# Kernel optimization log

Hardware: AMD Instinct MI355X
Metric: run time of the kernel (lower is better)

The kernel has to match this reference:

```python
import jax, jax.numpy as jnp
import numpy as np

NEG_SLOPE = 0.01  # nn.LeakyReLU default
NUM_GRAPHS = 64


def leaky_relu(x):
    return jnp.where(x >= 0, x, NEG_SLOPE * x)


def gcn_conv(x, edge_index, W, b):
    """PyG GCNConv: add self-loops, symmetric norm, aggregate, + bias."""
    n = x.shape[0]
    h = x @ W  # [N, F]
    loop = jnp.arange(n, dtype=edge_index.dtype)
    src = jnp.concatenate([edge_index[0], loop])
    dst = jnp.concatenate([edge_index[1], loop])
    deg = jax.ops.segment_sum(jnp.ones_like(dst, dtype=h.dtype), dst, num_segments=n)
    dinv = jnp.where(deg > 0, deg ** -0.5, 0.0)
    norm = dinv[src] * dinv[dst]  # [E+N]
    msg = h[src] * norm[:, None]  # [E+N, F] dominant intermediate
    out = jax.ops.segment_sum(msg, dst, num_segments=n)
    return out + b


def gep(x, batch, num_graphs):
    """global mean pool over batch segment ids."""
    s = jax.ops.segment_sum(x, batch, num_segments=num_graphs)
    cnt = jax.ops.segment_sum(jnp.ones(x.shape[0], dtype=x.dtype), batch, num_segments=num_graphs)
    return s / jnp.maximum(cnt, 1.0)[:, None]


def setup_inputs() -> dict:
    key = jax.random.key(0)
    ks = jax.random.split(key, 16)
    N, E, F, D, B = 10000, 80000, 1024, 128, NUM_GRAPHS
    sc = 1.0 / np.sqrt(F)
    inp = {
        "pro1_x": jax.random.normal(ks[0], (N, F), jnp.float32),
        "pro1_edge_index": jax.random.randint(ks[1], (2, E), 0, N, jnp.int64),
        "pro1_batch": jnp.sort(jax.random.randint(ks[2], (N,), 0, B, jnp.int64)),
        "pro2_x": jax.random.normal(ks[3], (N, F), jnp.float32),
        "pro2_edge_index": jax.random.randint(ks[4], (2, E), 0, N, jnp.int64),
        "pro2_batch": jnp.sort(jax.random.randint(ks[5], (N,), 0, B, jnp.int64)),
        "mas1_straight": 0, "mas1_flipped": 0, "mas2_straight": 0, "mas2_flipped": 0,
        "conv1_W": jax.random.normal(ks[6], (F, F), jnp.float32) * sc,
        "conv1_b": jnp.zeros((F,), jnp.float32),
        "fc1_W": jax.random.normal(ks[7], (F, D), jnp.float32) * sc,
        "fc1_b": jnp.zeros((D,), jnp.float32),
        "conv2_W": jax.random.normal(ks[8], (F, F), jnp.float32) * sc,
        "conv2_b": jnp.zeros((F,), jnp.float32),
        "fc2_W": jax.random.normal(ks[9], (F, D), jnp.float32) * sc,
        "fc2_b": jnp.zeros((D,), jnp.float32),
        "final_W": jax.random.normal(ks[10], (2 * D, 1), jnp.float32) * (1.0 / np.sqrt(2 * D)),
        "final_b": jnp.zeros((1,), jnp.float32),
    }
    return inp


def reference(pro1_x, pro1_edge_index, pro1_batch, pro2_x, pro2_edge_index, pro2_batch,
              mas1_straight, mas1_flipped, mas2_straight, mas2_flipped,
              conv1_W, conv1_b, fc1_W, fc1_b, conv2_W, conv2_b, fc2_W, fc2_b,
              final_W, final_b):
    # branch 1 (dropout = identity at inference)
    x = leaky_relu(gcn_conv(pro1_x, pro1_edge_index, conv1_W, conv1_b))
    x = gep(x, pro1_batch, NUM_GRAPHS)
    x = leaky_relu(x @ fc1_W + fc1_b)
    # branch 2
    xt = leaky_relu(gcn_conv(pro2_x, pro2_edge_index, conv2_W, conv2_b))
    xt = gep(xt, pro2_batch, NUM_GRAPHS)
    xt = leaky_relu(xt @ fc2_W + fc2_b)
    combined = jnp.concatenate([x, xt], axis=1)  # [B, 256]
    return combined @ final_W + final_b  # [B, 1]
```

## Files before the change

kernel.cpp:

```cpp
#include <hip/hip_runtime.h>
#include <cstdint>
#include <cstddef>

#define FDIM 1024
#define DDIM 128
#define NGRAPH 64
#define FCH 8
#define QN 4
#define FILLB 320

#define AS1 __attribute__((address_space(1)))
#define AS3 __attribute__((address_space(3)))

typedef float f32x4 __attribute__((ext_vector_type(4)));
typedef short s16x8 __attribute__((ext_vector_type(8)));

__device__ __forceinline__ unsigned short f2bf(float f) {
  unsigned int x = __float_as_uint(f);
  unsigned int r = (x + 0x7fffu + ((x >> 16) & 1u)) >> 16;
  return (unsigned short)r;
}
__device__ __forceinline__ float bflo(unsigned int v) {
  return __uint_as_float(v << 16);
}
__device__ __forceinline__ float bfhi(unsigned int v) {
  return __uint_as_float(v & 0xffff0000u);
}

__device__ __forceinline__ int lower_bound(const int* a, int n, int v) {
  int lo = 0, hi = n;
  while (lo < hi) {
    int mid = (lo + hi) >> 1;
    if (a[mid] < v) lo = mid + 1; else hi = mid;
  }
  return lo;
}
__global__ __launch_bounds__(256) void k_init(int* deg1, int* deg2,
                                              const int* __restrict__ batch1,
                                              const int* __restrict__ batch2,
                                              int* cnt1, int* gstart1,
                                              int* cnt2, int* gstart2, int N) {
  int bid = blockIdx.x, t = threadIdx.x;
  if (bid < 40) {
    int i = bid * 256 + t;
    if (i < N) deg1[i] = 1;
  } else if (bid < 80) {
    int i = (bid - 40) * 256 + t;
    if (i < N) deg2[i] = 1;
  } else {
    if (t < 128) {
      const int* batch = (t < NGRAPH) ? batch1 : batch2;
      int* cnt = (t < NGRAPH) ? cnt1 : cnt2;
      int* gstart = (t < NGRAPH) ? gstart1 : gstart2;
      int g = t & (NGRAPH - 1);
      int lo = lower_bound(batch, N, g);
      int hi = lower_bound(batch, N, g + 1);
      gstart[g] = lo;
      cnt[g] = hi - lo;
    }
  }
}

__global__ __launch_bounds__(256) void k_prep_cast(const int* __restrict__ ei1,
                                                   const int* __restrict__ ei2,
                                                   int* deg1, int* deg2,
                                                   const float4* __restrict__ x1,
                                                   const float4* __restrict__ x2,
                                                   const float* __restrict__ W1,
                                                   const float* __restrict__ W2,
                                                   ushort4* xb1, ushort4* xb2,
                                                   unsigned short* Wt1, unsigned short* Wt2,
                                                   int E, int n4, int gE, int nxb) {
  __shared__ unsigned short tile[64][65];
  int br = blockIdx.y;
  int x = blockIdx.x, t = threadIdx.x;
  if (x < gE) {
    const int* ei = br ? ei2 : ei1;
    int* deg = br ? deg2 : deg1;
    int i = x * 256 + t;
    if (i < E) atomicAdd(&deg[ei[E + i]], 1);
  } else if (x < gE + nxb) {
    const float4* xx = br ? x2 : x1;
    ushort4* xb = br ? xb2 : xb1;
    int i = (x - gE) * 256 + t;
    if (i < n4) {
      float4 v = xx[i];
      ushort4 o;
      o.x = f2bf(v.x); o.y = f2bf(v.y); o.z = f2bf(v.z); o.w = f2bf(v.w);
      xb[i] = o;
    }
  } else {
    const float* W = br ? W2 : W1;
    unsigned short* Wt = br ? Wt2 : Wt1;
    int tid16 = x - gE - nxb;
    int kb = tid16 >> 4, nb = tid16 & 15;
    int tn = t & 63, tg = t >> 6;
    #pragma unroll
    for (int r = 0; r < 16; ++r) {
      int kk = tg * 16 + r;
      tile[kk][tn] = f2bf(W[(size_t)(kb * 64 + kk) * FDIM + nb * 64 + tn]);
    }
    __syncthreads();
    #pragma unroll
    for (int r = 0; r < 16; ++r) {
      int nn = tg * 16 + r;
      Wt[(size_t)(nb * 64 + nn) * FDIM + kb * 64 + tn] = tile[tn][nn];
    }
  }
}

#define SCAN_T 1024
#define SCAN_PER 16
__global__ __launch_bounds__(SCAN_T) void k_scan(const int* __restrict__ deg1,
                                                 const int* __restrict__ deg2,
                                                 int* off1, int* off2,
                                                 int* cur1, int* cur2,
                                                 float* dinv1, float* dinv2, int n) {
  const int* deg = blockIdx.x ? deg2 : deg1;
  int* off = blockIdx.x ? off2 : off1;
  int* cur = blockIdx.x ? cur2 : cur1;
  float* dinv = blockIdx.x ? dinv2 : dinv1;
  __shared__ int sums[SCAN_T];
  int t = threadIdx.x;
  int base = t * SCAN_PER;
  int local[SCAN_PER];
  int s = 0;
  #pragma unroll
  for (int i = 0; i < SCAN_PER; ++i) {
    int idx = base + i;
    int d = (idx < n) ? deg[idx] : 0;
    local[i] = s;
    s += d;
    if (idx < n) dinv[idx] = rsqrtf((float)d);
  }
  sums[t] = s;
  __syncthreads();
  for (int o = 1; o < SCAN_T; o <<= 1) {
    int v = (t >= o) ? sums[t - o] : 0;
    __syncthreads();
    sums[t] += v;
    __syncthreads();
  }
  int basesum = (t > 0) ? sums[t - 1] : 0;
  #pragma unroll
  for (int i = 0; i < SCAN_PER; ++i) {
    int idx = base + i;
    if (idx < n) { int o = basesum + local[i]; off[idx] = o; cur[idx] = o; }
  }
  if (t == SCAN_T - 1) off[n] = sums[SCAN_T - 1];
}

__global__ __launch_bounds__(256) void k_fill_gemm(const int* __restrict__ ei1,
                                                   const int* __restrict__ ei2,
                                                   int* cur1, int* cur2,
                                                   const float* __restrict__ dinv1,
                                                   const float* __restrict__ dinv2,
                                                   int* adjsrc1, int* adjsrc2,
                                                   float* adjw1, float* adjw2,
                                                   const unsigned short* __restrict__ A1,
                                                   const unsigned short* __restrict__ A2,
                                                   const unsigned short* __restrict__ B1,
                                                   const unsigned short* __restrict__ B2,
                                                   unsigned short* __restrict__ C1,
                                                   unsigned short* __restrict__ C2,
                                                   int E, int N, int M) {
  __shared__ unsigned short sm[8192];
  int br = blockIdx.y;
  if (blockIdx.x < FILLB) {
    const int* ei = br ? ei2 : ei1;
    int* cur = br ? cur2 : cur1;
    const float* dinv = br ? dinv2 : dinv1;
    int* adjsrc = br ? adjsrc2 : adjsrc1;
    float* adjw = br ? adjw2 : adjw1;
    int i = blockIdx.x * 256 + threadIdx.x;
    if (i < E) {
      int s = ei[i];
      int d = ei[E + i];
      int p = atomicAdd(&cur[d], 1);
      adjsrc[p] = s;
      adjw[p] = dinv[s] * dinv[d];
    }
    if (i < N) {
      int p = atomicAdd(&cur[i], 1);
      adjsrc[p] = i;
      adjw[p] = dinv[i] * dinv[i];
    }
    return;
  }
  const unsigned short* A = br ? A2 : A1;
  const unsigned short* Bt = br ? B2 : B1;
  unsigned short* C = br ? C2 : C1;
  const int K = FDIM;
  int tid = threadIdx.x;
  int w = tid >> 6, lane = tid & 63;
  int wm = w >> 1, wn = w & 1;

  int bx = blockIdx.x - FILLB;
  int per_xcd = (gridDim.x - FILLB) >> 3;
  int l = (bx & 7) * per_xcd + (bx >> 3);
  int m0 = (l >> 3) * 128;
  int n0 = (l & 7) * 128;

  int sub = lane >> 2;
  int kq = lane & 3;

  f32x4 acc[4][4];
  #pragma unroll
  for (int i = 0; i < 4; ++i)
    #pragma unroll
    for (int j = 0; j < 4; ++j)
      acc[i][j] = (f32x4){0.f, 0.f, 0.f, 0.f};

  for (int k0 = 0; k0 < K; k0 += 32) {
    #pragma unroll
    for (int j = 0; j < 2; ++j) {
      int chunk = w * 2 + j;
      int ra = m0 + chunk * 16 + sub;
      if (ra > M - 1) ra = M - 1;
      const unsigned short* ga = A + (size_t)ra * K + k0 + kq * 8;
      __builtin_amdgcn_global_load_lds((const AS1 unsigned int*)ga,
                                       (AS3 unsigned int*)&sm[chunk * 512], 16, 0, 0);
      int rb = n0 + chunk * 16 + sub;
      const unsigned short* gb = Bt + (size_t)rb * K + k0 + kq * 8;
      __builtin_amdgcn_global_load_lds((const AS1 unsigned int*)gb,
                                       (AS3 unsigned int*)&sm[4096 + chunk * 512], 16, 0, 0);
    }
    __syncthreads();
    s16x8 af[4], bfr[4];
    #pragma unroll
    for (int i = 0; i < 4; ++i) {
      int rowa = wm * 64 + i * 16 + (lane & 15);
      af[i] = *(const s16x8*)&sm[rowa * 32 + (lane >> 4) * 8];
      int rowb = wn * 64 + i * 16 + (lane & 15);
      bfr[i] = *(const s16x8*)&sm[4096 + rowb * 32 + (lane >> 4) * 8];
    }
    #pragma unroll
    for (int i = 0; i < 4; ++i)
      #pragma unroll
      for (int j = 0; j < 4; ++j)
        acc[i][j] = __builtin_amdgcn_mfma_f32_16x16x32_bf16(af[i], bfr[j], acc[i][j], 0, 0, 0);
    __syncthreads();
  }

  #pragma unroll
  for (int i = 0; i < 4; ++i) {
    int row_base = m0 + wm * 64 + i * 16 + (lane >> 4) * 4;
    #pragma unroll
    for (int j = 0; j < 4; ++j) {
      int col = n0 + wn * 64 + j * 16 + (lane & 15);
      #pragma unroll
      for (int r = 0; r < 4; ++r) {
        int row = row_base + r;
        if (row < M) C[(size_t)row * FDIM + col] = f2bf(acc[i][j][r]);
      }
    }
  }
}

__global__ __launch_bounds__(256) void k_aggpool(const unsigned short* __restrict__ h1,
                                                 const unsigned short* __restrict__ h2,
                                                 const int* __restrict__ off1,
                                                 const int* __restrict__ off2,
                                                 const int* __restrict__ adjsrc1,
                                                 const int* __restrict__ adjsrc2,
                                                 const float* __restrict__ adjw1,
                                                 const float* __restrict__ adjw2,
                                                 const float* __restrict__ bias1,
                                                 const float* __restrict__ bias2,
                                                 const int* __restrict__ cnt1,
                                                 const int* __restrict__ cnt2,
                                                 const int* __restrict__ gstart1,
                                                 const int* __restrict__ gstart2,
                                                 float* pool4_1, float* pool4_2) {
  int br = blockIdx.y;
  const unsigned short* h = br ? h2 : h1;
  const int* off = br ? off2 : off1;
  const int* adjsrc = br ? adjsrc2 : adjsrc1;
  const float* adjw = br ? adjw2 : adjw1;
  const float* bias = br ? bias2 : bias1;
  const int* cnt = br ? cnt2 : cnt1;
  const int* gstart = br ? gstart2 : gstart1;
  float* pool4 = br ? pool4_2 : pool4_1;

  int x = blockIdx.x;
  int chunk = x & (FCH - 1);
  int r = x >> 3;
  int g = r & (NGRAPH - 1);
  int q = r >> 6;

  int t = threadIdx.x;
  int grp = t >> 6, lane = t & 63;

  int n = cnt[g];
  int start = gstart[g];
  int per = (n + QN - 1) / QN;
  int v0 = start + q * per;
  int v1 = min(start + n, v0 + per);

  int colbase = chunk * 128 + lane * 2;
  const unsigned short* hc = h + colbase;
  float2 b2 = *(const float2*)(bias + colbase);
  float s0 = 0.f, s1 = 0.f;

  for (int v = v0 + grp; v < v1; v += 4) {
    int pb = off[v], pe = off[v + 1];
    float a0 = 0.f, a1 = 0.f;
    for (int pbb = pb; pbb < pe; pbb += 64) {
      int m = min(64, pe - pbb);
      int lp = pbb + ((lane < m) ? lane : (m - 1));
      int vs = adjsrc[lp];
      float vw = adjw[lp];
      int j = 0;
      for (; j + 4 <= m; j += 4) {
        int i0 = __shfl(vs, j),     i1 = __shfl(vs, j + 1);
        int i2 = __shfl(vs, j + 2), i3 = __shfl(vs, j + 3);
        float w0 = __shfl(vw, j),     w1 = __shfl(vw, j + 1);
        float w2 = __shfl(vw, j + 2), w3 = __shfl(vw, j + 3);
        unsigned int h0 = *(const unsigned int*)(hc + ((size_t)i0 << 10));
        unsigned int hv1 = *(const unsigned int*)(hc + ((size_t)i1 << 10));
        unsigned int hv2 = *(const unsigned int*)(hc + ((size_t)i2 << 10));
        unsigned int hv3 = *(const unsigned int*)(hc + ((size_t)i3 << 10));
        a0 += w0 * bflo(h0);  a1 += w0 * bfhi(h0);
        a0 += w1 * bflo(hv1); a1 += w1 * bfhi(hv1);
        a0 += w2 * bflo(hv2); a1 += w2 * bfhi(hv2);
        a0 += w3 * bflo(hv3); a1 += w3 * bfhi(hv3);
      }
      for (; j < m; ++j) {
        int i0 = __shfl(vs, j);
        float w0 = __shfl(vw, j);
        unsigned int h0 = *(const unsigned int*)(hc + ((size_t)i0 << 10));
        a0 += w0 * bflo(h0);
        a1 += w0 * bfhi(h0);
      }
    }
    a0 += b2.x; a1 += b2.y;
    s0 += (a0 >= 0.f) ? a0 : 0.01f * a0;
    s1 += (a1 >= 0.f) ? a1 : 0.01f * a1;
  }

  __shared__ float sm[4][128];
  sm[grp][lane * 2] = s0;
  sm[grp][lane * 2 + 1] = s1;
  __syncthreads();
  if (t < 128) {
    float sum = sm[0][t] + sm[1][t] + sm[2][t] + sm[3][t];
    float ic = 1.0f / fmaxf((float)n, 1.0f);
    pool4[((size_t)(q * NGRAPH + g)) * FDIM + chunk * 128 + t] = sum * ic;
  }
}

__global__ __launch_bounds__(DDIM) void k_fc(const float* __restrict__ pool4_1,
                                             const float* __restrict__ pool4_2,
                                             const float* __restrict__ W1,
                                             const float* __restrict__ W2,
                                             const float* __restrict__ b1,
                                             const float* __restrict__ b2,
                                             float* out1, float* out2) {
  const float* pool4 = blockIdx.y ? pool4_2 : pool4_1;
  const float* W = blockIdx.y ? W2 : W1;
  const float* b = blockIdx.y ? b2 : b1;
  float* out = blockIdx.y ? out2 : out1;
  int g = blockIdx.x;
  int j = threadIdx.x;
  __shared__ float xs[FDIM];
  for (int k = j; k < FDIM; k += DDIM) {
    float v = 0.f;
    #pragma unroll
    for (int q = 0; q < QN; ++q)
      v += pool4[((size_t)(q * NGRAPH + g)) * FDIM + k];
    xs[k] = v;
  }
  __syncthreads();
  float acc = b[j];
  for (int k = 0; k < FDIM; ++k) acc += xs[k] * W[(size_t)k * DDIM + j];
  out[g * DDIM + j] = (acc >= 0.f) ? acc : 0.01f * acc;
}

__global__ __launch_bounds__(DDIM) void k_final(const float* __restrict__ o1,
                                                const float* __restrict__ o2,
                                                const float* __restrict__ W,
                                                const float* __restrict__ b,
                                                float* __restrict__ out) {
  int g = blockIdx.x;
  int t = threadIdx.x;
  float acc = o1[g * DDIM + t] * W[t] + o2[g * DDIM + t] * W[DDIM + t];
  #pragma unroll
  for (int o = 32; o > 0; o >>= 1) acc += __shfl_down(acc, o);
  __shared__ float ws2[2];
  if ((t & 63) == 0) ws2[t >> 6] = acc;
  __syncthreads();
  if (t == 0) out[g] = ws2[0] + ws2[1] + b[0];
}

extern "C" void kernel_launch(void* const* d_in, const int* in_sizes, int n_in,
                              void* d_out, int out_size, void* d_ws, size_t ws_size,
                              hipStream_t stream) {
  const float* x1 = (const float*)d_in[0];
  const int* ei1 = (const int*)d_in[1];
  const int* batch1 = (const int*)d_in[2];
  const float* x2 = (const float*)d_in[3];
  const int* ei2 = (const int*)d_in[4];
  const int* batch2 = (const int*)d_in[5];
  const float* conv1_W = (const float*)d_in[10];
  const float* conv1_b = (const float*)d_in[11];
  const float* fc1_W = (const float*)d_in[12];
  const float* fc1_b = (const float*)d_in[13];
  const float* conv2_W = (const float*)d_in[14];
  const float* conv2_b = (const float*)d_in[15];
  const float* fc2_W = (const float*)d_in[16];
  const float* fc2_b = (const float*)d_in[17];
  const float* final_W = (const float*)d_in[18];
  const float* final_b = (const float*)d_in[19];
  float* out = (float*)d_out;

  const int N = in_sizes[2];
  const int E = in_sizes[1] / 2;
  const int A = E + N;

  size_t off_b = 0;
  auto alloc = [&](size_t bytes) -> void* {
    void* p = (char*)d_ws + off_b;
    off_b += (bytes + 255) & ~(size_t)255;
    return p;
  };
  unsigned short* xbf1 = (unsigned short*)alloc((size_t)N * FDIM * 2);
  unsigned short* xbf2 = (unsigned short*)alloc((size_t)N * FDIM * 2);
  unsigned short* hbf1 = (unsigned short*)alloc((size_t)N * FDIM * 2);
  unsigned short* hbf2 = (unsigned short*)alloc((size_t)N * FDIM * 2);
  unsigned short* Wt1 = (unsigned short*)alloc((size_t)FDIM * FDIM * 2);
  unsigned short* Wt2 = (unsigned short*)alloc((size_t)FDIM * FDIM * 2);
  int* deg1 = (int*)alloc(N * 4);
  int* deg2 = (int*)alloc(N * 4);
  int* cnt1 = (int*)alloc(NGRAPH * 4);
  int* cnt2 = (int*)alloc(NGRAPH * 4);
  int* gstart1 = (int*)alloc(NGRAPH * 4);
  int* gstart2 = (int*)alloc(NGRAPH * 4);
  int* off1 = (int*)alloc((N + 1) * 4);
  int* off2 = (int*)alloc((N + 1) * 4);
  int* cur1 = (int*)alloc(N * 4);
  int* cur2 = (int*)alloc(N * 4);
  float* dinv1 = (float*)alloc(N * 4);
  float* dinv2 = (float*)alloc(N * 4);
  int* adjsrc1 = (int*)alloc((size_t)A * 4);
  int* adjsrc2 = (int*)alloc((size_t)A * 4);
  float* adjw1 = (float*)alloc((size_t)A * 4);
  float* adjw2 = (float*)alloc((size_t)A * 4);
  float* pool4_1 = (float*)alloc((size_t)QN * NGRAPH * FDIM * 4);
  float* pool4_2 = (float*)alloc((size_t)QN * NGRAPH * FDIM * 4);
  float* fco1 = (float*)alloc(NGRAPH * DDIM * 4);
  float* fco2 = (float*)alloc(NGRAPH * DDIM * 4);

  const int T = 256;
  int gE = (E + T - 1) / T;
  int n4 = N * FDIM / 4;
  int nxb = (n4 + T - 1) / T;
  int mt = (N + 127) / 128;
  dim3 gPrepCast(gE + nxb + 256, 2);
  dim3 gFillGemm(FILLB + mt * 8, 2);
  dim3 gAgg(FCH * NGRAPH * QN, 2);
  dim3 gFc(NGRAPH, 2);

  k_init<<<81, T, 0, stream>>>(deg1, deg2, batch1, batch2,
                               cnt1, gstart1, cnt2, gstart2, N);
  k_prep_cast<<<gPrepCast, T, 0, stream>>>(ei1, ei2, deg1, deg2,
                                           (const float4*)x1, (const float4*)x2,
                                           conv1_W, conv2_W,
                                           (ushort4*)xbf1, (ushort4*)xbf2, Wt1, Wt2,
                                           E, n4, gE, nxb);
  k_scan<<<2, SCAN_T, 0, stream>>>(deg1, deg2, off1, off2, cur1, cur2, dinv1, dinv2, N);
  k_fill_gemm<<<gFillGemm, T, 0, stream>>>(ei1, ei2, cur1, cur2, dinv1, dinv2,
                                           adjsrc1, adjsrc2, adjw1, adjw2,
                                           xbf1, xbf2, Wt1, Wt2, hbf1, hbf2,
                                           E, N, N);
  k_aggpool<<<gAgg, T, 0, stream>>>(hbf1, hbf2, off1, off2, adjsrc1, adjsrc2,
                                    adjw1, adjw2, conv1_b, conv2_b,
                                    cnt1, cnt2, gstart1, gstart2, pool4_1, pool4_2);
  k_fc<<<gFc, DDIM, 0, stream>>>(pool4_1, pool4_2, fc1_W, fc2_W, fc1_b, fc2_b, fco1, fco2);
  k_final<<<NGRAPH, DDIM, 0, stream>>>(fco1, fco2, final_W, final_b, out);
}
```

Baseline: 333.1 us.

## Stagger branch pipelines so GEMM of one branch overlaps cast/agg of the other

Restructures the kernel schedule so branch 2's input/weight cast runs alongside branch 1's GEMM, and branch 2's GEMM runs alongside branch 1's aggregation-pool, instead of running both branches in lockstep. The FC and final-linear kernels are also merged into one heads kernel, removing a launch and an intermediate buffer. The aim is to fill the GPU with heterogeneous work (compute-bound GEMM plus memory-bound cast and gather) and cut launch count. The risk is that the GEMM on the critical path now covers only half the tiles per launch, so it fills the GPU less, and mixed block types may be unbalanced.

```diff
diff --git a/kernel.cpp b/kernel.cpp
--- a/kernel.cpp
+++ b/kernel.cpp
@@ -7,7 +7,7 @@
 #define NGRAPH 64
 #define FCH 8
 #define QN 4
-#define FILLB 320
+#define AGGB (FCH * NGRAPH * QN)
 
 #define AS1 __attribute__((address_space(1)))
 #define AS3 __attribute__((address_space(3)))
@@ -27,176 +27,18 @@
   return __uint_as_float(v & 0xffff0000u);
 }
 
-__device__ __forceinline__ int lower_bound(const int* a, int n, int v) {
-  int lo = 0, hi = n;
-  while (lo < hi) {
-    int mid = (lo + hi) >> 1;
-    if (a[mid] < v) lo = mid + 1; else hi = mid;
-  }
-  return lo;
-}
-__global__ __launch_bounds__(256) void k_init(int* deg1, int* deg2,
-                                              const int* __restrict__ batch1,
-                                              const int* __restrict__ batch2,
-                                              int* cnt1, int* gstart1,
-                                              int* cnt2, int* gstart2, int N) {
-  int bid = blockIdx.x, t = threadIdx.x;
-  if (bid < 40) {
-    int i = bid * 256 + t;
-    if (i < N) deg1[i] = 1;
-  } else if (bid < 80) {
-    int i = (bid - 40) * 256 + t;
-    if (i < N) deg2[i] = 1;
-  } else {
-    if (t < 128) {
-      const int* batch = (t < NGRAPH) ? batch1 : batch2;
-      int* cnt = (t < NGRAPH) ? cnt1 : cnt2;
-      int* gstart = (t < NGRAPH) ? gstart1 : gstart2;
-      int g = t & (NGRAPH - 1);
-      int lo = lower_bound(batch, N, g);
-      int hi = lower_bound(batch, N, g + 1);
-      gstart[g] = lo;
-      cnt[g] = hi - lo;
-    }
-  }
-}
-
-__global__ __launch_bounds__(256) void k_prep_cast(const int* __restrict__ ei1,
-                                                   const int* __restrict__ ei2,
-                                                   int* deg1, int* deg2,
-                                                   const float4* __restrict__ x1,
-                                                   const float4* __restrict__ x2,
-                                                   const float* __restrict__ W1,
-                                                   const float* __restrict__ W2,
-                                                   ushort4* xb1, ushort4* xb2,
-                                                   unsigned short* Wt1, unsigned short* Wt2,
-                                                   int E, int n4, int gE, int nxb) {
-  __shared__ unsigned short tile[64][65];
-  int br = blockIdx.y;
-  int x = blockIdx.x, t = threadIdx.x;
-  if (x < gE) {
-    const int* ei = br ? ei2 : ei1;
-    int* deg = br ? deg2 : deg1;
-    int i = x * 256 + t;
-    if (i < E) atomicAdd(&deg[ei[E + i]], 1);
-  } else if (x < gE + nxb) {
-    const float4* xx = br ? x2 : x1;
-    ushort4* xb = br ? xb2 : xb1;
-    int i = (x - gE) * 256 + t;
-    if (i < n4) {
-      float4 v = xx[i];
-      ushort4 o;
-      o.x = f2bf(v.x); o.y = f2bf(v.y); o.z = f2bf(v.z); o.w = f2bf(v.w);
-      xb[i] = o;
-    }
-  } else {
-    const float* W = br ? W2 : W1;
-    unsigned short* Wt = br ? Wt2 : Wt1;
-    int tid16 = x - gE - nxb;
-    int kb = tid16 >> 4, nb = tid16 & 15;
-    int tn = t & 63, tg = t >> 6;
-    #pragma unroll
-    for (int r = 0; r < 16; ++r) {
-      int kk = tg * 16 + r;
-      tile[kk][tn] = f2bf(W[(size_t)(kb * 64 + kk) * FDIM + nb * 64 + tn]);
-    }
-    __syncthreads();
-    #pragma unroll
-    for (int r = 0; r < 16; ++r) {
-      int nn = tg * 16 + r;
-      Wt[(size_t)(nb * 64 + nn) * FDIM + kb * 64 + tn] = tile[tn][nn];
-    }
-  }
-}
-
-#define SCAN_T 1024
-#define SCAN_PER 16
-__global__ __launch_bounds__(SCAN_T) void k_scan(const int* __restrict__ deg1,
-                                                 const int* __restrict__ deg2,
-                                                 int* off1, int* off2,
-                                                 int* cur1, int* cur2,
-                                                 float* dinv1, float* dinv2, int n) {
-  const int* deg = blockIdx.x ? deg2 : deg1;
-  int* off = blockIdx.x ? off2 : off1;
-  int* cur = blockIdx.x ? cur2 : cur1;
-  float* dinv = blockIdx.x ? dinv2 : dinv1;
-  __shared__ int sums[SCAN_T];
-  int t = threadIdx.x;
-  int base = t * SCAN_PER;
-  int local[SCAN_PER];
-  int s = 0;
-  #pragma unroll
-  for (int i = 0; i < SCAN_PER; ++i) {
-    int idx = base + i;
-    int d = (idx < n) ? deg[idx] : 0;
-    local[i] = s;
-    s += d;
-    if (idx < n) dinv[idx] = rsqrtf((float)d);
-  }
-  sums[t] = s;
-  __syncthreads();
-  for (int o = 1; o < SCAN_T; o <<= 1) {
-    int v = (t >= o) ? sums[t - o] : 0;
-    __syncthreads();
-    sums[t] += v;
-    __syncthreads();
-  }
-  int basesum = (t > 0) ? sums[t - 1] : 0;
-  #pragma unroll
-  for (int i = 0; i < SCAN_PER; ++i) {
-    int idx = base + i;
-    if (idx < n) { int o = basesum + local[i]; off[idx] = o; cur[idx] = o; }
-  }
-  if (t == SCAN_T - 1) off[n] = sums[SCAN_T - 1];
-}
-
-__global__ __launch_bounds__(256) void k_fill_gemm(const int* __restrict__ ei1,
-                                                   const int* __restrict__ ei2,
-                                                   int* cur1, int* cur2,
-                                                   const float* __restrict__ dinv1,
-                                                   const float* __restrict__ dinv2,
-                                                   int* adjsrc1, int* adjsrc2,
-                                                   float* adjw1, float* adjw2,
-                                                   const unsigned short* __restrict__ A1,
-                                                   const unsigned short* __restrict__ A2,
-                                                   const unsigned short* __restrict__ B1,
-                                                   const unsigned short* __restrict__ B2,
-                                                   unsigned short* __restrict__ C1,
-                                                   unsigned short* __restrict__ C2,
-                                                   int E, int N, int M) {
+
+__device__ __forceinline__ void dev_gemm(const unsigned short* __restrict__ A,
+                                         const unsigned short* __restrict__ Bt,
+                                         unsigned short* __restrict__ C,
+                                         int M, int bx, int gemmBlocks) {
   __shared__ unsigned short sm[8192];
-  int br = blockIdx.y;
-  if (blockIdx.x < FILLB) {
-    const int* ei = br ? ei2 : ei1;
-    int* cur = br ? cur2 : cur1;
-    const float* dinv = br ? dinv2 : dinv1;
-    int* adjsrc = br ? adjsrc2 : adjsrc1;
-    float* adjw = br ? adjw2 : adjw1;
-    int i = blockIdx.x * 256 + threadIdx.x;
-    if (i < E) {
-      int s = ei[i];
-      int d = ei[E + i];
-      int p = atomicAdd(&cur[d], 1);
-      adjsrc[p] = s;
-      adjw[p] = dinv[s] * dinv[d];
-    }
-    if (i < N) {
-      int p = atomicAdd(&cur[i], 1);
-      adjsrc[p] = i;
-      adjw[p] = dinv[i] * dinv[i];
-    }
-    return;
-  }
-  const unsigned short* A = br ? A2 : A1;
-  const unsigned short* Bt = br ? B2 : B1;
-  unsigned short* C = br ? C2 : C1;
   const int K = FDIM;
   int tid = threadIdx.x;
   int w = tid >> 6, lane = tid & 63;
   int wm = w >> 1, wn = w & 1;
 
-  int bx = blockIdx.x - FILLB;
-  int per_xcd = (gridDim.x - FILLB) >> 3;
+  int per_xcd = gemmBlocks >> 3;
   int l = (bx & 7) * per_xcd + (bx >> 3);
   int m0 = (l >> 3) * 128;
   int n0 = (l & 7) * 128;
@@ -257,34 +99,62 @@
   }
 }
 
-__global__ __launch_bounds__(256) void k_aggpool(const unsigned short* __restrict__ h1,
-                                                 const unsigned short* __restrict__ h2,
-                                                 const int* __restrict__ off1,
-                                                 const int* __restrict__ off2,
-                                                 const int* __restrict__ adjsrc1,
-                                                 const int* __restrict__ adjsrc2,
-                                                 const float* __restrict__ adjw1,
-                                                 const float* __restrict__ adjw2,
-                                                 const float* __restrict__ bias1,
-                                                 const float* __restrict__ bias2,
-                                                 const int* __restrict__ cnt1,
-                                                 const int* __restrict__ cnt2,
-                                                 const int* __restrict__ gstart1,
-                                                 const int* __restrict__ gstart2,
-                                                 float* pool4_1, float* pool4_2) {
-  int br = blockIdx.y;
-  const unsigned short* h = br ? h2 : h1;
-  const int* off = br ? off2 : off1;
-  const int* adjsrc = br ? adjsrc2 : adjsrc1;
-  const float* adjw = br ? adjw2 : adjw1;
-  const float* bias = br ? bias2 : bias1;
-  const int* cnt = br ? cnt2 : cnt1;
-  const int* gstart = br ? gstart2 : gstart1;
-  float* pool4 = br ? pool4_2 : pool4_1;
-
-  int x = blockIdx.x;
-  int chunk = x & (FCH - 1);
-  int r = x >> 3;
+__device__ __forceinline__ void dev_fill(const int* __restrict__ ei, int* cur,
+                                         const float* __restrict__ dinv,
+                                         int* adjsrc, float* adjw, int E, int N, int i) {
+  if (i < E) {
+    int s = ei[i];
+    int d = ei[E + i];
+    int p = atomicAdd(&cur[d], 1);
+    adjsrc[p] = s;
+    adjw[p] = dinv[s] * dinv[d];
+  }
+  if (i < N) {
+    int p = atomicAdd(&cur[i], 1);
+    adjsrc[p] = i;
+    adjw[p] = dinv[i] * dinv[i];
+  }
+}
+
+__device__ __forceinline__ void dev_cast_x(const float4* __restrict__ x,
+                                           ushort4* xb, int i, int n4) {
+  if (i < n4) {
+    float4 v = x[i];
+    ushort4 o;
+    o.x = f2bf(v.x); o.y = f2bf(v.y); o.z = f2bf(v.z); o.w = f2bf(v.w);
+    xb[i] = o;
+  }
+}
+
+__device__ __forceinline__ void dev_cast_w(const float* __restrict__ W,
+                                           unsigned short* Wt, int tid16) {
+  __shared__ unsigned short tile[64][65];
+  int t = threadIdx.x;
+  int kb = tid16 >> 4, nb = tid16 & 15;
+  int tn = t & 63, tg = t >> 6;
+  #pragma unroll
+  for (int r = 0; r < 16; ++r) {
+    int kk = tg * 16 + r;
+    tile[kk][tn] = f2bf(W[(size_t)(kb * 64 + kk) * FDIM + nb * 64 + tn]);
+  }
+  __syncthreads();
+  #pragma unroll
+  for (int r = 0; r < 16; ++r) {
+    int nn = tg * 16 + r;
+    Wt[(size_t)(nb * 64 + nn) * FDIM + kb * 64 + tn] = tile[tn][nn];
+  }
+}
+
+__device__ __forceinline__ void dev_aggpool(const unsigned short* __restrict__ h,
+                                            const int* __restrict__ off,
+                                            const int* __restrict__ adjsrc,
+                                            const float* __restrict__ adjw,
+                                            const float* __restrict__ bias,
+                                            const int* __restrict__ cnt,
+                                            const int* __restrict__ gstart,
+                                            float* pool4, int a) {
+  int chunk = a & (FCH - 1);
+  int r = a >> 3;
   int g = r & (NGRAPH - 1);
   int q = r >> 6;
 
@@ -338,28 +208,181 @@
     s1 += (a1 >= 0.f) ? a1 : 0.01f * a1;
   }
 
-  __shared__ float sm[4][128];
-  sm[grp][lane * 2] = s0;
-  sm[grp][lane * 2 + 1] = s1;
+  __shared__ float smr[4][128];
+  smr[grp][lane * 2] = s0;
+  smr[grp][lane * 2 + 1] = s1;
   __syncthreads();
   if (t < 128) {
-    float sum = sm[0][t] + sm[1][t] + sm[2][t] + sm[3][t];
+    float sum = smr[0][t] + smr[1][t] + smr[2][t] + smr[3][t];
     float ic = 1.0f / fmaxf((float)n, 1.0f);
     pool4[((size_t)(q * NGRAPH + g)) * FDIM + chunk * 128 + t] = sum * ic;
   }
 }
 
-__global__ __launch_bounds__(DDIM) void k_fc(const float* __restrict__ pool4_1,
-                                             const float* __restrict__ pool4_2,
-                                             const float* __restrict__ W1,
-                                             const float* __restrict__ W2,
-                                             const float* __restrict__ b1,
-                                             const float* __restrict__ b2,
-                                             float* out1, float* out2) {
-  const float* pool4 = blockIdx.y ? pool4_2 : pool4_1;
-  const float* W = blockIdx.y ? W2 : W1;
-  const float* b = blockIdx.y ? b2 : b1;
-  float* out = blockIdx.y ? out2 : out1;
+
+__device__ __forceinline__ int lower_bound(const int* a, int n, int v) {
+  int lo = 0, hi = n;
+  while (lo < hi) {
+    int mid = (lo + hi) >> 1;
+    if (a[mid] < v) lo = mid + 1; else hi = mid;
+  }
+  return lo;
+}
+__global__ __launch_bounds__(256) void k_init(int* deg1, int* deg2,
+                                              const int* __restrict__ batch1,
+                                              const int* __restrict__ batch2,
+                                              int* cnt1, int* gstart1,
+                                              int* cnt2, int* gstart2, int N) {
+  int bid = blockIdx.x, t = threadIdx.x;
+  if (bid < 40) {
+    int i = bid * 256 + t;
+    if (i < N) deg1[i] = 1;
+  } else if (bid < 80) {
+    int i = (bid - 40) * 256 + t;
+    if (i < N) deg2[i] = 1;
+  } else {
+    if (t < 128) {
+      const int* batch = (t < NGRAPH) ? batch1 : batch2;
+      int* cnt = (t < NGRAPH) ? cnt1 : cnt2;
+      int* gstart = (t < NGRAPH) ? gstart1 : gstart2;
+      int g = t & (NGRAPH - 1);
+      int lo = lower_bound(batch, N, g);
+      int hi = lower_bound(batch, N, g + 1);
+      gstart[g] = lo;
+      cnt[g] = hi - lo;
+    }
+  }
+}
+
+__global__ __launch_bounds__(256) void k_prep_cast1(const int* __restrict__ ei1,
+                                                    const int* __restrict__ ei2,
+                                                    int* deg1, int* deg2,
+                                                    const float4* __restrict__ x1,
+                                                    const float* __restrict__ W1,
+                                                    ushort4* xb1, unsigned short* Wt1,
+                                                    int E, int n4, int gE, int nxb) {
+  int x = blockIdx.x, t = threadIdx.x;
+  if (x < 2 * gE) {
+    int br = x >= gE;
+    const int* ei = br ? ei2 : ei1;
+    int* deg = br ? deg2 : deg1;
+    int i = (x - br * gE) * 256 + t;
+    if (i < E) atomicAdd(&deg[ei[E + i]], 1);
+  } else if (x < 2 * gE + nxb) {
+    dev_cast_x(x1, xb1, (x - 2 * gE) * 256 + t, n4);
+  } else {
+    dev_cast_w(W1, Wt1, x - 2 * gE - nxb);
+  }
+}
+
+#define SCAN_T 1024
+#define SCAN_PER 16
+__global__ __launch_bounds__(SCAN_T) void k_scan(const int* __restrict__ deg1,
+                                                 const int* __restrict__ deg2,
+                                                 int* off1, int* off2,
+                                                 int* cur1, int* cur2,
+                                                 float* dinv1, float* dinv2, int n) {
+  const int* deg = blockIdx.x ? deg2 : deg1;
+  int* off = blockIdx.x ? off2 : off1;
+  int* cur = blockIdx.x ? cur2 : cur1;
+  float* dinv = blockIdx.x ? dinv2 : dinv1;
+  __shared__ int sums[SCAN_T];
+  int t = threadIdx.x;
+  int base = t * SCAN_PER;
+  int local[SCAN_PER];
+  int s = 0;
+  #pragma unroll
+  for (int i = 0; i < SCAN_PER; ++i) {
+    int idx = base + i;
+    int d = (idx < n) ? deg[idx] : 0;
+    local[i] = s;
+    s += d;
+    if (idx < n) dinv[idx] = rsqrtf((float)d);
+  }
+  sums[t] = s;
+  __syncthreads();
+  for (int o = 1; o < SCAN_T; o <<= 1) {
+    int v = (t >= o) ? sums[t - o] : 0;
+    __syncthreads();
+    sums[t] += v;
+    __syncthreads();
+  }
+  int basesum = (t > 0) ? sums[t - 1] : 0;
+  #pragma unroll
+  for (int i = 0; i < SCAN_PER; ++i) {
+    int idx = base + i;
+    if (idx < n) { int o = basesum + local[i]; off[idx] = o; cur[idx] = o; }
+  }
+  if (t == SCAN_T - 1) off[n] = sums[SCAN_T - 1];
+}
+
+__global__ __launch_bounds__(256) void k_gemm1_fill_cast2(
+    const unsigned short* __restrict__ A1, const unsigned short* __restrict__ B1,
+    unsigned short* __restrict__ C1,
+    const int* __restrict__ ei1, const int* __restrict__ ei2,
+    int* cur1, int* cur2,
+    const float* __restrict__ dinv1, const float* __restrict__ dinv2,
+    int* adjsrc1, int* adjsrc2, float* adjw1, float* adjw2,
+    const float4* __restrict__ x2, const float* __restrict__ W2,
+    ushort4* xb2, unsigned short* Wt2,
+    int E, int N, int n4, int gE, int nxb, int GB) {
+  int x = blockIdx.x, t = threadIdx.x;
+  if (x < GB) {
+    dev_gemm(A1, B1, C1, N, x, GB);
+    return;
+  }
+  int y = x - GB;
+  if (y < 2 * gE) {
+    int br = y >= gE;
+    dev_fill(br ? ei2 : ei1, br ? cur2 : cur1, br ? dinv2 : dinv1,
+             br ? adjsrc2 : adjsrc1, br ? adjw2 : adjw1, E, N,
+             (y - br * gE) * 256 + t);
+    return;
+  }
+  int z = y - 2 * gE;
+  if (z < nxb) {
+    dev_cast_x(x2, xb2, z * 256 + t, n4);
+  } else {
+    dev_cast_w(W2, Wt2, z - nxb);
+  }
+}
+
+__global__ __launch_bounds__(256) void k_gemm2_agg1(
+    const unsigned short* __restrict__ A2, const unsigned short* __restrict__ B2,
+    unsigned short* __restrict__ C2,
+    const unsigned short* __restrict__ h1,
+    const int* __restrict__ off1, const int* __restrict__ adjsrc1,
+    const float* __restrict__ adjw1, const float* __restrict__ bias1,
+    const int* __restrict__ cnt1, const int* __restrict__ gstart1,
+    float* pool4_1, int N, int GB) {
+  int x = blockIdx.x;
+  if (x < GB) {
+    dev_gemm(A2, B2, C2, N, x, GB);
+  } else {
+    dev_aggpool(h1, off1, adjsrc1, adjw1, bias1, cnt1, gstart1, pool4_1, x - GB);
+  }
+}
+
+__global__ __launch_bounds__(256) void k_agg2(const unsigned short* __restrict__ h2,
+                                              const int* __restrict__ off2,
+                                              const int* __restrict__ adjsrc2,
+                                              const float* __restrict__ adjw2,
+                                              const float* __restrict__ bias2,
+                                              const int* __restrict__ cnt2,
+                                              const int* __restrict__ gstart2,
+                                              float* pool4_2) {
+  dev_aggpool(h2, off2, adjsrc2, adjw2, bias2, cnt2, gstart2, pool4_2, blockIdx.x);
+}
+
+__global__ __launch_bounds__(DDIM) void k_heads(const float* __restrict__ pool4_1,
+                                                const float* __restrict__ pool4_2,
+                                                const float* __restrict__ W1,
+                                                const float* __restrict__ W2,
+                                                const float* __restrict__ b1,
+                                                const float* __restrict__ b2,
+                                                const float* __restrict__ fW,
+                                                const float* __restrict__ fb,
+                                                float* __restrict__ out) {
   int g = blockIdx.x;
   int j = threadIdx.x;
   __shared__ float xs[FDIM];
@@ -367,29 +390,32 @@
     float v = 0.f;
     #pragma unroll
     for (int q = 0; q < QN; ++q)
-      v += pool4[((size_t)(q * NGRAPH + g)) * FDIM + k];
+      v += pool4_1[((size_t)(q * NGRAPH + g)) * FDIM + k];
     xs[k] = v;
   }
   __syncthreads();
-  float acc = b[j];
-  for (int k = 0; k < FDIM; ++k) acc += xs[k] * W[(size_t)k * DDIM + j];
-  out[g * DDIM + j] = (acc >= 0.f) ? acc : 0.01f * acc;
-}
-
-__global__ __launch_bounds__(DDIM) void k_final(const float* __restrict__ o1,
-                                                const float* __restrict__ o2,
-                                                const float* __restrict__ W,
-                                                const float* __restrict__ b,
-                                                float* __restrict__ out) {
-  int g = blockIdx.x;
-  int t = threadIdx.x;
-  float acc = o1[g * DDIM + t] * W[t] + o2[g * DDIM + t] * W[DDIM + t];
-  #pragma unroll
-  for (int o = 32; o > 0; o >>= 1) acc += __shfl_down(acc, o);
+  float acc1 = b1[j];
+  for (int k = 0; k < FDIM; ++k) acc1 += xs[k] * W1[(size_t)k * DDIM + j];
+  acc1 = (acc1 >= 0.f) ? acc1 : 0.01f * acc1;
+  __syncthreads();
+  for (int k = j; k < FDIM; k += DDIM) {
+    float v = 0.f;
+    #pragma unroll
+    for (int q = 0; q < QN; ++q)
+      v += pool4_2[((size_t)(q * NGRAPH + g)) * FDIM + k];
+    xs[k] = v;
+  }
+  __syncthreads();
+  float acc2 = b2[j];
+  for (int k = 0; k < FDIM; ++k) acc2 += xs[k] * W2[(size_t)k * DDIM + j];
+  acc2 = (acc2 >= 0.f) ? acc2 : 0.01f * acc2;
+  float part = acc1 * fW[j] + acc2 * fW[DDIM + j];
+  #pragma unroll
+  for (int o = 32; o > 0; o >>= 1) part += __shfl_down(part, o);
   __shared__ float ws2[2];
-  if ((t & 63) == 0) ws2[t >> 6] = acc;
-  __syncthreads();
-  if (t == 0) out[g] = ws2[0] + ws2[1] + b[0];
+  if ((j & 63) == 0) ws2[j >> 6] = part;
+  __syncthreads();
+  if (j == 0) out[g] = ws2[0] + ws2[1] + fb[0];
 }
 
 extern "C" void kernel_launch(void* const* d_in, const int* in_sizes, int n_in,
@@ -447,34 +473,31 @@
   float* adjw2 = (float*)alloc((size_t)A * 4);
   float* pool4_1 = (float*)alloc((size_t)QN * NGRAPH * FDIM * 4);
   float* pool4_2 = (float*)alloc((size_t)QN * NGRAPH * FDIM * 4);
-  float* fco1 = (float*)alloc(NGRAPH * DDIM * 4);
-  float* fco2 = (float*)alloc(NGRAPH * DDIM * 4);
 
   const int T = 256;
   int gE = (E + T - 1) / T;
   int n4 = N * FDIM / 4;
   int nxb = (n4 + T - 1) / T;
   int mt = (N + 127) / 128;
-  dim3 gPrepCast(gE + nxb + 256, 2);
-  dim3 gFillGemm(FILLB + mt * 8, 2);
-  dim3 gAgg(FCH * NGRAPH * QN, 2);
-  dim3 gFc(NGRAPH, 2);
+  int GB = mt * 8;
 
   k_init<<<81, T, 0, stream>>>(deg1, deg2, batch1, batch2,
                                cnt1, gstart1, cnt2, gstart2, N);
-  k_prep_cast<<<gPrepCast, T, 0, stream>>>(ei1, ei2, deg1, deg2,
-                                           (const float4*)x1, (const float4*)x2,
-                                           conv1_W, conv2_W,
-                                           (ushort4*)xbf1, (ushort4*)xbf2, Wt1, Wt2,
-                                           E, n4, gE, nxb);
+  k_prep_cast1<<<2 * gE + nxb + 256, T, 0, stream>>>(ei1, ei2, deg1, deg2,
+                                                     (const float4*)x1, conv1_W,
+                                                     (ushort4*)xbf1, Wt1,
+                                                     E, n4, gE, nxb);
   k_scan<<<2, SCAN_T, 0, stream>>>(deg1, deg2, off1, off2, cur1, cur2, dinv1, dinv2, N);
-  k_fill_gemm<<<gFillGemm, T, 0, stream>>>(ei1, ei2, cur1, cur2, dinv1, dinv2,
-                                           adjsrc1, adjsrc2, adjw1, adjw2,
-                                           xbf1, xbf2, Wt1, Wt2, hbf1, hbf2,
-                                           E, N, N);
-  k_aggpool<<<gAgg, T, 0, stream>>>(hbf1, hbf2, off1, off2, adjsrc1, adjsrc2,
-                                    adjw1, adjw2, conv1_b, conv2_b,
-                                    cnt1, cnt2, gstart1, gstart2, pool4_1, pool4_2);
-  k_fc<<<gFc, DDIM, 0, stream>>>(pool4_1, pool4_2, fc1_W, fc2_W, fc1_b, fc2_b, fco1, fco2);
-  k_final<<<NGRAPH, DDIM, 0, stream>>>(fco1, fco2, final_W, final_b, out);
-}
+  k_gemm1_fill_cast2<<<GB + 2 * gE + nxb + 256, T, 0, stream>>>(
+      xbf1, Wt1, hbf1,
+      ei1, ei2, cur1, cur2, dinv1, dinv2, adjsrc1, adjsrc2, adjw1, adjw2,
+      (const float4*)x2, conv2_W, (ushort4*)xbf2, Wt2,
+      E, N, n4, gE, nxb, GB);
+  k_gemm2_agg1<<<GB + AGGB, T, 0, stream>>>(
+      xbf2, Wt2, hbf2,
+      hbf1, off1, adjsrc1, adjw1, conv1_b, cnt1, gstart1, pool4_1, N, GB);
+  k_agg2<<<AGGB, T, 0, stream>>>(hbf2, off2, adjsrc2, adjw2, conv2_b,
+                                 cnt2, gstart2, pool4_2);
+  k_heads<<<NGRAPH, DDIM, 0, stream>>>(pool4_1, pool4_2, fc1_W, fc2_W,
+                                       fc1_b, fc2_b, final_W, final_b, out);
+}
```

After: 376.7 us. +13.1%, slower.
